# Kernel tuning notes

Hardware: AMD Instinct MI355X
Metric: run time of the kernel (lower is better)

The kernel has to match this reference:

```python
import jax, jax.numpy as jnp
import numpy as np

N_CONS, N_VARS, N_EDGES, N_CAND = 100000, 200000, 8000000, 20000
C_FEAT, V_FEAT = 5, 19


def setup_inputs() -> dict:
    key = jax.random.key(0)
    k1, k2, k3, k4, k5, k6 = jax.random.split(key, 6)
    constraint = jax.random.normal(k1, (N_CONS, C_FEAT), dtype=jnp.float32)
    variable = jax.random.normal(k2, (N_VARS, V_FEAT), dtype=jnp.float32)
    c_edge_index = jax.random.randint(k3, (N_EDGES,), 0, N_CONS, dtype=jnp.int64)
    v_edge_index = jax.random.randint(k4, (N_EDGES,), 0, N_VARS, dtype=jnp.int64)
    cv_edge_index = jnp.stack([c_edge_index, v_edge_index], axis=0)  # [2, E]
    edge_attr = jax.random.normal(k5, (N_EDGES,), dtype=jnp.float32)
    cand_mask = jax.random.randint(k6, (N_CAND,), 0, N_VARS, dtype=jnp.int64)
    return {
        "constraint": constraint,
        "variable": variable,
        "cv_edge_index": cv_edge_index,
        "edge_attr": edge_attr,
        "cand_mask": cand_mask,
    }


def reference(constraint, variable, cv_edge_index, edge_attr, cand_mask):
    # Expression encoded in from_expression:
    #   variable_1_5   = variable[:, 5][v_edge_index]       (gather var feat to edges)
    #   constraint_1_2 = constraint[:, 2][c_edge_index]     (gather cons feat to edges)
    #   msg   = variable_1_5 * edge_attr + constraint_1_2   (edge elementwise)
    #   agg   = scatter_sum(msg, v_edge_index, n_vars)      (scatter to variables)
    #   res   = agg * variable[:, 0] + sqrt(abs(variable[:, 3]))
    #   return res[cand_mask]
    c_edge_index = cv_edge_index[0]
    v_edge_index = cv_edge_index[1]
    variable_1_5 = variable[:, 5][v_edge_index]      # [E]
    constraint_1_2 = constraint[:, 2][c_edge_index]  # [E]
    msg = variable_1_5 * edge_attr + constraint_1_2  # [E]
    agg = jax.ops.segment_sum(msg, v_edge_index, num_segments=variable.shape[0])  # [n_vars]
    result = agg * variable[:, 0] + jnp.sqrt(jnp.abs(variable[:, 3]))
    return result[cand_mask]
```

## Files before the change

### kernel.cpp

```cpp
#include <hip/hip_runtime.h>
#include <math.h>

#define N_CONS  100000
#define N_VARS  200000
#define N_EDGES 8000000
#define N_CAND  20000
#define C_FEAT  5
#define V_FEAT  19
#define BM_WORDS      6250
#define BM_WORDS_PAD  6400
#define ACC_SLOTS     20000
#define EDGE_BLOCKS   256
#define KSLICES       8
#define KS_LEN        (EDGE_BLOCKS / KSLICES)
#define CID_BLOCKS    ((ACC_SLOTS + 255) / 256)

__global__ void pack_kernel(const float* __restrict__ variable,
                            const float* __restrict__ constraint,
                            const int* __restrict__ cand,
                            float* __restrict__ var5,
                            float* __restrict__ cons2,
                            unsigned int* __restrict__ bitmap) {
    int i = blockIdx.x * blockDim.x + threadIdx.x;
    if (i < N_VARS) var5[i]  = variable[i * V_FEAT + 5];
    if (i < N_CONS) cons2[i] = constraint[i * C_FEAT + 2];
    if (i < N_CAND) {
        int v = cand[i];
        atomicOr(&bitmap[v >> 5], 1u << (v & 31));
    }
}

__global__ void __launch_bounds__(1024)
scan_kernel(const unsigned int* __restrict__ bitmap,
            uint2* __restrict__ bp) {
    __shared__ unsigned int wsum[16];
    const int CH = 7;
    int t = threadIdx.x;
    int lane = t & 63, wid = t >> 6;
    int base = t * CH;
    unsigned int w_loc[CH];
    unsigned int pf_loc[CH];
    unsigned int sum = 0;
#pragma unroll
    for (int j = 0; j < CH; ++j) {
        int w = base + j;
        unsigned int word = (w < BM_WORDS_PAD) ? bitmap[w] : 0u;
        w_loc[j]  = word;
        pf_loc[j] = sum;
        sum += __popc(word);
    }
    unsigned int inc = sum;
#pragma unroll
    for (int off = 1; off < 64; off <<= 1) {
        unsigned int n = __shfl_up(inc, off, 64);
        if (lane >= off) inc += n;
    }
    if (lane == 63) wsum[wid] = inc;
    __syncthreads();
    if (wid == 0 && lane < 16) {
        unsigned int v = wsum[lane];
#pragma unroll
        for (int off = 1; off < 16; off <<= 1) {
            unsigned int n = __shfl_up(v, off, 16);
            if (lane >= off) v += n;
        }
        wsum[lane] = v;
    }
    __syncthreads();
    unsigned int ebase = inc - sum + (wid ? wsum[wid - 1] : 0u);
#pragma unroll
    for (int j = 0; j < CH; ++j) {
        int w = base + j;
        if (w < BM_WORDS_PAD) bp[w] = make_uint2(w_loc[j], ebase + pf_loc[j]);
    }
}

__global__ void __launch_bounds__(1024)
edge_kernel(const int* __restrict__ c_idx,
            const int* __restrict__ v_idx,
            const float* __restrict__ edge_attr,
            const float* __restrict__ var5,
            const float* __restrict__ cons2,
            const uint2* __restrict__ bp,
            float* __restrict__ partials) {
    __shared__ uint2 lds_bp[BM_WORDS_PAD];
    __shared__ float lds_acc[ACC_SLOTS];

    {
        const uint4* src = (const uint4*)bp;
        uint4* dst = (uint4*)lds_bp;
        for (int j = threadIdx.x; j < BM_WORDS_PAD / 2; j += blockDim.x)
            dst[j] = src[j];
        for (int j = threadIdx.x; j < ACC_SLOTS; j += blockDim.x)
            lds_acc[j] = 0.0f;
    }
    __syncthreads();

    const int nch = N_EDGES / 8;
    int stride = gridDim.x * blockDim.x;
    const int4*   v4 = (const int4*)v_idx;
    const int4*   c4 = (const int4*)c_idx;
    const float4* e4 = (const float4*)edge_attr;

    for (int g = blockIdx.x * blockDim.x + threadIdx.x; g < nch; g += stride) {
        int4   va = v4[2 * g],     vb = v4[2 * g + 1];
        int4   ca = c4[2 * g],     cb = c4[2 * g + 1];
        float4 ea = e4[2 * g],     eb = e4[2 * g + 1];

#define PROC(vv, cc, ee)                                                     \
        {                                                                    \
            uint2 e2 = lds_bp[(vv) >> 5];                                    \
            if ((e2.x >> ((vv) & 31)) & 1u) {                                \
                int cid = (int)e2.y +                                        \
                          __popc(e2.x & ((1u << ((vv) & 31)) - 1u));         \
                atomicAdd(&lds_acc[cid],                                     \
                          var5[vv] * (ee) + cons2[cc]);                      \
            }                                                                \
        }
        PROC(va.x, ca.x, ea.x)  PROC(va.y, ca.y, ea.y)
        PROC(va.z, ca.z, ea.z)  PROC(va.w, ca.w, ea.w)
        PROC(vb.x, cb.x, eb.x)  PROC(vb.y, cb.y, eb.y)
        PROC(vb.z, cb.z, eb.z)  PROC(vb.w, cb.w, eb.w)
#undef PROC
    }
    __syncthreads();

    {
        float4* dst = (float4*)(partials + (size_t)blockIdx.x * ACC_SLOTS);
        const float4* src = (const float4*)lds_acc;
        for (int j = threadIdx.x; j < ACC_SLOTS / 4; j += blockDim.x)
            dst[j] = src[j];
    }
}

__global__ void reduce1_kernel(const float* __restrict__ partials,
                               float* __restrict__ p2) {
    int cb = blockIdx.x % CID_BLOCKS;
    int ks = blockIdx.x / CID_BLOCKS;
    int cid = cb * 256 + threadIdx.x;
    if (cid >= ACC_SLOTS) return;
    float acc = 0.0f;
#pragma unroll
    for (int k = 0; k < KS_LEN; ++k)
        acc += partials[(size_t)(ks * KS_LEN + k) * ACC_SLOTS + cid];
    p2[(size_t)ks * ACC_SLOTS + cid] = acc;
}

__global__ void out_kernel(const int* __restrict__ cand,
                           const float* __restrict__ p2,
                           const uint2* __restrict__ bp,
                           const float* __restrict__ variable,
                           float* __restrict__ out) {
    int i = blockIdx.x * blockDim.x + threadIdx.x;
    if (i >= N_CAND) return;
    int v = cand[i];
    uint2 e2 = bp[v >> 5];
    int cid = (int)e2.y + __popc(e2.x & ((1u << (v & 31)) - 1u));
    float acc = 0.0f;
#pragma unroll
    for (int s = 0; s < KSLICES; ++s)
        acc += p2[(size_t)s * ACC_SLOTS + cid];
    out[i] = acc * variable[v * V_FEAT + 0] + sqrtf(fabsf(variable[v * V_FEAT + 3]));
}

extern "C" void kernel_launch(void* const* d_in, const int* in_sizes, int n_in,
                              void* d_out, int out_size, void* d_ws, size_t ws_size,
                              hipStream_t stream) {
    const float* constraint = (const float*)d_in[0];
    const float* variable   = (const float*)d_in[1];
    const int*   cv_edge    = (const int*)d_in[2];
    const float* edge_attr  = (const float*)d_in[3];
    const int*   cand_mask  = (const int*)d_in[4];
    float* out = (float*)d_out;

    const int* c_idx = cv_edge;
    const int* v_idx = cv_edge + N_EDGES;

    float* var5  = (float*)d_ws;
    float* cons2 = var5 + N_VARS;
    unsigned int* bitmap = (unsigned int*)(cons2 + N_CONS);
    uint2* bp            = (uint2*)(bitmap + BM_WORDS_PAD);
    float* partials      = (float*)(bp + BM_WORDS_PAD);
    float* p2            = partials + (size_t)EDGE_BLOCKS * ACC_SLOTS;

    hipMemsetAsync(bitmap, 0, BM_WORDS_PAD * sizeof(unsigned int), stream);

    {
        int threads = 256;
        int blocks = (N_VARS + threads - 1) / threads;
        pack_kernel<<<blocks, threads, 0, stream>>>(variable, constraint, cand_mask,
                                                    var5, cons2, bitmap);
    }
    scan_kernel<<<1, 1024, 0, stream>>>(bitmap, bp);
    edge_kernel<<<EDGE_BLOCKS, 1024, 0, stream>>>(c_idx, v_idx, edge_attr,
                                                  var5, cons2, bp, partials);
    reduce1_kernel<<<CID_BLOCKS * KSLICES, 256, 0, stream>>>(partials, p2);
    {
        int threads = 256;
        int blocks = (N_CAND + threads - 1) / threads;
        out_kernel<<<blocks, threads, 0, stream>>>(cand_mask, p2, bp, variable, out);
    }
}
```

Measured before the change: 57.42 us.

## Split edge pass into wave-compaction and separate LDS-atomic accumulation kernels

The fused edge kernel is replaced by two stages. First, a compaction kernel streams the edges, keeps only those hitting candidate variables, and writes (cid, msg) records into per-wave regions using ballot and prefix popcount. Second, an accumulation kernel with 128 blocks sums those records into LDS with atomics, and a single reduce pass folds the 128 partials. Dropping the 80KB accumulator from the streaming kernel lowers its LDS use, allowing more resident blocks per CU and a smaller partials buffer. The cost is an extra kernel launch and a global write and read of the compacted records.

```diff
diff --git a/kernel.cpp b/kernel.cpp
--- a/kernel.cpp
+++ b/kernel.cpp
@@ -10,9 +10,11 @@
 #define BM_WORDS      6250
 #define BM_WORDS_PAD  6400
 #define ACC_SLOTS     20000
-#define EDGE_BLOCKS   256
-#define KSLICES       8
-#define KS_LEN        (EDGE_BLOCKS / KSLICES)
+#define CMP_BLOCKS    512
+#define WAVES_TOTAL   (CMP_BLOCKS * 1024 / 64)
+#define REGION_STRIDE 1024
+#define ACC_BLOCKS    128
+#define REGIONS_PER_BLOCK (WAVES_TOTAL / ACC_BLOCKS)
 #define CID_BLOCKS    ((ACC_SLOTS + 255) / 256)
 
 __global__ void pack_kernel(const float* __restrict__ variable,
@@ -75,79 +77,98 @@
     }
 }
 
-__global__ void __launch_bounds__(1024)
-edge_kernel(const int* __restrict__ c_idx,
-            const int* __restrict__ v_idx,
-            const float* __restrict__ edge_attr,
-            const float* __restrict__ var5,
-            const float* __restrict__ cons2,
-            const uint2* __restrict__ bp,
-            float* __restrict__ partials) {
+__global__ void __launch_bounds__(1024, 8)
+compact_kernel(const int* __restrict__ c_idx,
+               const int* __restrict__ v_idx,
+               const float* __restrict__ edge_attr,
+               const float* __restrict__ var5,
+               const float* __restrict__ cons2,
+               const uint2* __restrict__ bp,
+               uint2* __restrict__ recs,
+               int* __restrict__ wcount) {
     __shared__ uint2 lds_bp[BM_WORDS_PAD];
-    __shared__ float lds_acc[ACC_SLOTS];
-
     {
         const uint4* src = (const uint4*)bp;
         uint4* dst = (uint4*)lds_bp;
         for (int j = threadIdx.x; j < BM_WORDS_PAD / 2; j += blockDim.x)
             dst[j] = src[j];
-        for (int j = threadIdx.x; j < ACC_SLOTS; j += blockDim.x)
-            lds_acc[j] = 0.0f;
-    }
-    __syncthreads();
-
-    const int nch = N_EDGES / 8;
-    int stride = gridDim.x * blockDim.x;
-    const int4*   v4 = (const int4*)v_idx;
-    const int4*   c4 = (const int4*)c_idx;
-    const float4* e4 = (const float4*)edge_attr;
+    }
+    __syncthreads();
+
+    const int nch = N_EDGES / 4;
+    const int stride = gridDim.x * blockDim.x;
+    const int lane = threadIdx.x & 63;
+    const unsigned long long lt = (1ull << lane) - 1ull;
+    const int wgid = (blockIdx.x * blockDim.x + threadIdx.x) >> 6;
+    uint2* region = recs + (size_t)wgid * REGION_STRIDE;
+    int woff = 0;
 
     for (int g = blockIdx.x * blockDim.x + threadIdx.x; g < nch; g += stride) {
-        int4   va = v4[2 * g],     vb = v4[2 * g + 1];
-        int4   ca = c4[2 * g],     cb = c4[2 * g + 1];
-        float4 ea = e4[2 * g],     eb = e4[2 * g + 1];
-
-#define PROC(vv, cc, ee)                                                     \
+        int4   v = ((const int4*)v_idx)[g];
+        int4   c = ((const int4*)c_idx)[g];
+        float4 e = ((const float4*)edge_attr)[g];
+
+#define SLOT(vv, cc, ee)                                                     \
         {                                                                    \
             uint2 e2 = lds_bp[(vv) >> 5];                                    \
-            if ((e2.x >> ((vv) & 31)) & 1u) {                                \
+            bool keep = (e2.x >> ((vv) & 31)) & 1u;                          \
+            unsigned long long m = __ballot(keep);                           \
+            if (keep) {                                                      \
                 int cid = (int)e2.y +                                        \
                           __popc(e2.x & ((1u << ((vv) & 31)) - 1u));         \
-                atomicAdd(&lds_acc[cid],                                     \
-                          var5[vv] * (ee) + cons2[cc]);                      \
+                float msg = var5[vv] * (ee) + cons2[cc];                     \
+                region[woff + __popcll(m & lt)] =                            \
+                    make_uint2((unsigned)cid, __float_as_uint(msg));         \
             }                                                                \
+            woff += __popcll(m);                                             \
         }
-        PROC(va.x, ca.x, ea.x)  PROC(va.y, ca.y, ea.y)
-        PROC(va.z, ca.z, ea.z)  PROC(va.w, ca.w, ea.w)
-        PROC(vb.x, cb.x, eb.x)  PROC(vb.y, cb.y, eb.y)
-        PROC(vb.z, cb.z, eb.z)  PROC(vb.w, cb.w, eb.w)
-#undef PROC
-    }
-    __syncthreads();
-
-    {
-        float4* dst = (float4*)(partials + (size_t)blockIdx.x * ACC_SLOTS);
-        const float4* src = (const float4*)lds_acc;
-        for (int j = threadIdx.x; j < ACC_SLOTS / 4; j += blockDim.x)
-            dst[j] = src[j];
-    }
-}
-
-__global__ void reduce1_kernel(const float* __restrict__ partials,
-                               float* __restrict__ p2) {
-    int cb = blockIdx.x % CID_BLOCKS;
-    int ks = blockIdx.x / CID_BLOCKS;
-    int cid = cb * 256 + threadIdx.x;
+        SLOT(v.x, c.x, e.x)  SLOT(v.y, c.y, e.y)
+        SLOT(v.z, c.z, e.z)  SLOT(v.w, c.w, e.w)
+#undef SLOT
+    }
+    if (lane == 0) wcount[wgid] = woff;
+}
+
+__global__ void __launch_bounds__(1024, 4)
+accum_kernel(const uint2* __restrict__ recs,
+             const int* __restrict__ wcount,
+             float* __restrict__ partials) {
+    __shared__ float acc[ACC_SLOTS];
+    for (int j = threadIdx.x; j < ACC_SLOTS; j += 1024) acc[j] = 0.0f;
+    __syncthreads();
+
+    int sub = threadIdx.x >> 7;
+    int idx = threadIdx.x & 127;
+    for (int rr = 0; rr < REGIONS_PER_BLOCK; rr += 8) {
+        int r = blockIdx.x * REGIONS_PER_BLOCK + rr + sub;
+        int cnt = wcount[r];
+        const uint2* region = recs + (size_t)r * REGION_STRIDE;
+        for (int i = idx; i < cnt; i += 128) {
+            uint2 rec = region[i];
+            atomicAdd(&acc[rec.x], __uint_as_float(rec.y));
+        }
+    }
+    __syncthreads();
+
+    float4* dst = (float4*)(partials + (size_t)blockIdx.x * ACC_SLOTS);
+    const float4* src = (const float4*)acc;
+    for (int j = threadIdx.x; j < ACC_SLOTS / 4; j += 1024)
+        dst[j] = src[j];
+}
+
+__global__ void reduce_kernel(const float* __restrict__ partials,
+                              float* __restrict__ agg2) {
+    int cid = blockIdx.x * 256 + threadIdx.x;
     if (cid >= ACC_SLOTS) return;
-    float acc = 0.0f;
-#pragma unroll
-    for (int k = 0; k < KS_LEN; ++k)
-        acc += partials[(size_t)(ks * KS_LEN + k) * ACC_SLOTS + cid];
-    p2[(size_t)ks * ACC_SLOTS + cid] = acc;
+    float s = 0.0f;
+#pragma unroll 8
+    for (int k = 0; k < ACC_BLOCKS; ++k)
+        s += partials[(size_t)k * ACC_SLOTS + cid];
+    agg2[cid] = s;
 }
 
 __global__ void out_kernel(const int* __restrict__ cand,
-                           const float* __restrict__ p2,
+                           const float* __restrict__ agg2,
                            const uint2* __restrict__ bp,
                            const float* __restrict__ variable,
                            float* __restrict__ out) {
@@ -156,11 +177,7 @@
     int v = cand[i];
     uint2 e2 = bp[v >> 5];
     int cid = (int)e2.y + __popc(e2.x & ((1u << (v & 31)) - 1u));
-    float acc = 0.0f;
-#pragma unroll
-    for (int s = 0; s < KSLICES; ++s)
-        acc += p2[(size_t)s * ACC_SLOTS + cid];
-    out[i] = acc * variable[v * V_FEAT + 0] + sqrtf(fabsf(variable[v * V_FEAT + 3]));
+    out[i] = agg2[cid] * variable[v * V_FEAT + 0] + sqrtf(fabsf(variable[v * V_FEAT + 3]));
 }
 
 extern "C" void kernel_launch(void* const* d_in, const int* in_sizes, int n_in,
@@ -180,8 +197,10 @@
     float* cons2 = var5 + N_VARS;
     unsigned int* bitmap = (unsigned int*)(cons2 + N_CONS);
     uint2* bp            = (uint2*)(bitmap + BM_WORDS_PAD);
-    float* partials      = (float*)(bp + BM_WORDS_PAD);
-    float* p2            = partials + (size_t)EDGE_BLOCKS * ACC_SLOTS;
+    int*   wcount        = (int*)(bp + BM_WORDS_PAD);
+    float* agg2          = (float*)(wcount + WAVES_TOTAL);
+    float* partials      = agg2 + ACC_SLOTS;
+    uint2* recs          = (uint2*)(partials + (size_t)ACC_BLOCKS * ACC_SLOTS);
 
     hipMemsetAsync(bitmap, 0, BM_WORDS_PAD * sizeof(unsigned int), stream);
 
@@ -192,12 +211,13 @@
                                                     var5, cons2, bitmap);
     }
     scan_kernel<<<1, 1024, 0, stream>>>(bitmap, bp);
-    edge_kernel<<<EDGE_BLOCKS, 1024, 0, stream>>>(c_idx, v_idx, edge_attr,
-                                                  var5, cons2, bp, partials);
-    reduce1_kernel<<<CID_BLOCKS * KSLICES, 256, 0, stream>>>(partials, p2);
+    compact_kernel<<<CMP_BLOCKS, 1024, 0, stream>>>(c_idx, v_idx, edge_attr,
+                                                    var5, cons2, bp, recs, wcount);
+    accum_kernel<<<ACC_BLOCKS, 1024, 0, stream>>>(recs, wcount, partials);
+    reduce_kernel<<<CID_BLOCKS, 256, 0, stream>>>(partials, agg2);
     {
         int threads = 256;
         int blocks = (N_CAND + threads - 1) / threads;
-        out_kernel<<<blocks, threads, 0, stream>>>(cand_mask, p2, bp, variable, out);
-    }
-}
+        out_kernel<<<blocks, threads, 0, stream>>>(cand_mask, agg2, bp, variable, out);
+    }
+}
```

Result: slower. 66.33 us (+15.5%).

## Batch edge gathers before LDS atomics and collapse reduction to single pass

Applied to the files above, without the earlier changes.

Restructures the edge loop so all eight bitmap lookups run first, then all eight gathers from var5 and cons2, then the LDS atomics. A scheduling barrier keeps the gathers from being interleaved with the atomics, which exposes more memory-level parallelism. Gathers for edges that are filtered out are redirected to index 0 so the loads can be issued without branching. The two-level partial reduction becomes one kernel that sums all 256 partials per slot, with only 79 blocks, and launch_bounds gains a min-blocks hint that adds register pressure.

```diff
diff --git a/kernel.cpp b/kernel.cpp
--- a/kernel.cpp
+++ b/kernel.cpp
@@ -7,12 +7,9 @@
 #define N_CAND  20000
 #define C_FEAT  5
 #define V_FEAT  19
-#define BM_WORDS      6250
 #define BM_WORDS_PAD  6400
 #define ACC_SLOTS     20000
 #define EDGE_BLOCKS   256
-#define KSLICES       8
-#define KS_LEN        (EDGE_BLOCKS / KSLICES)
 #define CID_BLOCKS    ((ACC_SLOTS + 255) / 256)
 
 __global__ void pack_kernel(const float* __restrict__ variable,
@@ -75,7 +72,7 @@
     }
 }
 
-__global__ void __launch_bounds__(1024)
+__global__ void __launch_bounds__(1024, 4)
 edge_kernel(const int* __restrict__ c_idx,
             const int* __restrict__ v_idx,
             const float* __restrict__ edge_attr,
@@ -97,31 +94,42 @@
     __syncthreads();
 
     const int nch = N_EDGES / 8;
-    int stride = gridDim.x * blockDim.x;
+    const int stride = gridDim.x * blockDim.x;
     const int4*   v4 = (const int4*)v_idx;
     const int4*   c4 = (const int4*)c_idx;
     const float4* e4 = (const float4*)edge_attr;
 
     for (int g = blockIdx.x * blockDim.x + threadIdx.x; g < nch; g += stride) {
-        int4   va = v4[2 * g],     vb = v4[2 * g + 1];
-        int4   ca = c4[2 * g],     cb = c4[2 * g + 1];
-        float4 ea = e4[2 * g],     eb = e4[2 * g + 1];
-
-#define PROC(vv, cc, ee)                                                     \
-        {                                                                    \
-            uint2 e2 = lds_bp[(vv) >> 5];                                    \
-            if ((e2.x >> ((vv) & 31)) & 1u) {                                \
-                int cid = (int)e2.y +                                        \
-                          __popc(e2.x & ((1u << ((vv) & 31)) - 1u));         \
-                atomicAdd(&lds_acc[cid],                                     \
-                          var5[vv] * (ee) + cons2[cc]);                      \
-            }                                                                \
-        }
-        PROC(va.x, ca.x, ea.x)  PROC(va.y, ca.y, ea.y)
-        PROC(va.z, ca.z, ea.z)  PROC(va.w, ca.w, ea.w)
-        PROC(vb.x, cb.x, eb.x)  PROC(vb.y, cb.y, eb.y)
-        PROC(vb.z, cb.z, eb.z)  PROC(vb.w, cb.w, eb.w)
-#undef PROC
+        int4   va = v4[2 * g],  vb = v4[2 * g + 1];
+        int4   ca = c4[2 * g],  cb = c4[2 * g + 1];
+        float4 ea = e4[2 * g],  eb = e4[2 * g + 1];
+
+        int   vv[8] = { va.x, va.y, va.z, va.w, vb.x, vb.y, vb.z, vb.w };
+        int   cc[8] = { ca.x, ca.y, ca.z, ca.w, cb.x, cb.y, cb.z, cb.w };
+        float ee[8] = { ea.x, ea.y, ea.z, ea.w, eb.x, eb.y, eb.z, eb.w };
+
+        bool keep[8];
+        int  cid[8];
+#pragma unroll
+        for (int k = 0; k < 8; ++k) {
+            uint2 e2 = lds_bp[vv[k] >> 5];
+            keep[k] = (e2.x >> (vv[k] & 31)) & 1u;
+            cid[k]  = (int)e2.y + __popc(e2.x & ((1u << (vv[k] & 31)) - 1u));
+        }
+
+        float v5[8], c2[8];
+#pragma unroll
+        for (int k = 0; k < 8; ++k) {
+            v5[k] = var5[keep[k] ? vv[k] : 0];
+            c2[k] = cons2[keep[k] ? cc[k] : 0];
+        }
+        __builtin_amdgcn_sched_barrier(0);
+
+#pragma unroll
+        for (int k = 0; k < 8; ++k) {
+            if (keep[k])
+                atomicAdd(&lds_acc[cid[k]], v5[k] * ee[k] + c2[k]);
+        }
     }
     __syncthreads();
 
@@ -133,21 +141,19 @@
     }
 }
 
-__global__ void reduce1_kernel(const float* __restrict__ partials,
-                               float* __restrict__ p2) {
-    int cb = blockIdx.x % CID_BLOCKS;
-    int ks = blockIdx.x / CID_BLOCKS;
-    int cid = cb * 256 + threadIdx.x;
+__global__ void reduce_kernel(const float* __restrict__ partials,
+                              float* __restrict__ agg2) {
+    int cid = blockIdx.x * 256 + threadIdx.x;
     if (cid >= ACC_SLOTS) return;
-    float acc = 0.0f;
-#pragma unroll
-    for (int k = 0; k < KS_LEN; ++k)
-        acc += partials[(size_t)(ks * KS_LEN + k) * ACC_SLOTS + cid];
-    p2[(size_t)ks * ACC_SLOTS + cid] = acc;
+    float s = 0.0f;
+#pragma unroll 8
+    for (int k = 0; k < EDGE_BLOCKS; ++k)
+        s += partials[(size_t)k * ACC_SLOTS + cid];
+    agg2[cid] = s;
 }
 
 __global__ void out_kernel(const int* __restrict__ cand,
-                           const float* __restrict__ p2,
+                           const float* __restrict__ agg2,
                            const uint2* __restrict__ bp,
                            const float* __restrict__ variable,
                            float* __restrict__ out) {
@@ -156,11 +162,7 @@
     int v = cand[i];
     uint2 e2 = bp[v >> 5];
     int cid = (int)e2.y + __popc(e2.x & ((1u << (v & 31)) - 1u));
-    float acc = 0.0f;
-#pragma unroll
-    for (int s = 0; s < KSLICES; ++s)
-        acc += p2[(size_t)s * ACC_SLOTS + cid];
-    out[i] = acc * variable[v * V_FEAT + 0] + sqrtf(fabsf(variable[v * V_FEAT + 3]));
+    out[i] = agg2[cid] * variable[v * V_FEAT + 0] + sqrtf(fabsf(variable[v * V_FEAT + 3]));
 }
 
 extern "C" void kernel_launch(void* const* d_in, const int* in_sizes, int n_in,
@@ -181,7 +183,7 @@
     unsigned int* bitmap = (unsigned int*)(cons2 + N_CONS);
     uint2* bp            = (uint2*)(bitmap + BM_WORDS_PAD);
     float* partials      = (float*)(bp + BM_WORDS_PAD);
-    float* p2            = partials + (size_t)EDGE_BLOCKS * ACC_SLOTS;
+    float* agg2          = partials + (size_t)EDGE_BLOCKS * ACC_SLOTS;
 
     hipMemsetAsync(bitmap, 0, BM_WORDS_PAD * sizeof(unsigned int), stream);
 
@@ -194,10 +196,10 @@
     scan_kernel<<<1, 1024, 0, stream>>>(bitmap, bp);
     edge_kernel<<<EDGE_BLOCKS, 1024, 0, stream>>>(c_idx, v_idx, edge_attr,
                                                   var5, cons2, bp, partials);
-    reduce1_kernel<<<CID_BLOCKS * KSLICES, 256, 0, stream>>>(partials, p2);
+    reduce_kernel<<<CID_BLOCKS, 256, 0, stream>>>(partials, agg2);
     {
         int threads = 256;
         int blocks = (N_CAND + threads - 1) / threads;
-        out_kernel<<<blocks, threads, 0, stream>>>(cand_mask, p2, bp, variable, out);
-    }
-}
+        out_kernel<<<blocks, threads, 0, stream>>>(cand_mask, agg2, bp, variable, out);
+    }
+}
```

New measurement: 61.18 us. 1.07x slower.
